# Kernel tuning notes

Hardware: AMD Instinct MI355X
Metric: run time of the kernel (lower is better)

The kernel has to match this reference:

```python
import jax, jax.numpy as jnp
import numpy as np

N, C, T = 8, 256, 512
H, KQ, OUT = 8, 256, 256
EPS = 1e-5


def sym_linear(x, w, stride):
    # w: (2, out_dim); circulant-grouped expansion to (2T, out_dim), then x @ cp
    out_dim = w.shape[1]
    idx = (jnp.arange(out_dim)[None, :] - jnp.arange(T)[:, None] * stride) % out_dim  # (T, out_dim)
    cp = w[:, idx].transpose(1, 0, 2).reshape(2 * T, out_dim)  # cat of rolled copies
    return x @ cp


def ln2d(x, g, b):
    # LayerNorm over last two dims (T, 2T) with affine params (T, 2T)
    mu = jnp.mean(x, axis=(-2, -1), keepdims=True)
    var = jnp.mean(jnp.square(x - mu), axis=(-2, -1), keepdims=True)
    return (x - mu) / jnp.sqrt(var + EPS) * g + b


def setup_inputs() -> dict:
    key = jax.random.key(0)
    ks = jax.random.split(key, 16)
    stdv = 1.0 / np.sqrt(2 * T)
    u = lambda k, shape, s: jax.random.uniform(k, shape, jnp.float32, -s, s)
    return {
        "x": jax.random.normal(ks[0], (N, C, T), jnp.float32),
        "Wq": u(ks[1], (KQ, C), 1.0 / np.sqrt(C)),
        "Wk": u(ks[2], (KQ, C), 1.0 / np.sqrt(C)),
        "Wv": u(ks[3], (OUT, C), 1.0 / np.sqrt(C)),
        "m1w0": u(ks[4], (2, 2 * T), stdv),
        "m2w0": u(ks[5], (2, 2 * T), stdv),
        "m1w1": u(ks[6], (2, 2 * T), stdv),
        "m2w1": u(ks[7], (2, T), stdv),
        "ln1g0": 1.0 + 0.1 * jax.random.normal(ks[8], (T, 2 * T), jnp.float32),
        "ln1b0": 0.1 * jax.random.normal(ks[9], (T, 2 * T), jnp.float32),
        "ln2g0": 1.0 + 0.1 * jax.random.normal(ks[10], (T, 2 * T), jnp.float32),
        "ln2b0": 0.1 * jax.random.normal(ks[11], (T, 2 * T), jnp.float32),
        "ln1g1": 1.0 + 0.1 * jax.random.normal(ks[12], (T, 2 * T), jnp.float32),
        "ln1b1": 0.1 * jax.random.normal(ks[13], (T, 2 * T), jnp.float32),
    }


def reference(x, Wq, Wk, Wv, m1w0, m2w0, m1w1, m2w1,
              ln1g0, ln1b0, ln2g0, ln2b0, ln1g1, ln1b1):
    dk = KQ // H
    q = jnp.einsum('oc,nct->not', Wq, x).reshape(N, H, dk, T).transpose(0, 1, 3, 2)  # (N,H,T,dk)
    k = jnp.einsum('oc,nct->not', Wk, x).reshape(N, H, dk, T)                        # (N,H,dk,T)
    v = jnp.einsum('oc,nct->not', Wv, x).reshape(N, H, OUT // H, T).transpose(0, 1, 3, 2)  # (N,H,T,dv)

    scores = jnp.einsum('nhtd,nhds->nhts', q, k) / np.sqrt(dk)  # (N,H,T,T)
    ar = jnp.arange(T, dtype=jnp.float32)
    pd = jnp.abs(ar[None, :] - ar[:, None]) / (T - 1)  # (T,T)
    p = jnp.stack([scores, jnp.broadcast_to(pd, scores.shape)], axis=-1)  # (N,H,T,T,2)
    p = p.reshape(N, H, T, 2 * T)

    def transpose_pairs(z):
        return z.reshape(N, H, T, T, 2).transpose(0, 1, 3, 2, 4)

    # mix block 0 (intermediate)
    p = ln2d(sym_linear(p, m1w0, 2), ln1g0, ln1b0)
    p = jax.nn.gelu(transpose_pairs(p), approximate=False).reshape(N, H, T, 2 * T)
    p = ln2d(sym_linear(p, m2w0, 2), ln2g0, ln2b0)
    p = jax.nn.gelu(transpose_pairs(p), approximate=False).reshape(N, H, T, 2 * T)

    # mix block 1 (final)
    p = ln2d(sym_linear(p, m1w1, 2), ln1g1, ln1b1)
    p = jax.nn.gelu(transpose_pairs(p), approximate=False).reshape(N, H, T, 2 * T)
    p = sym_linear(p, m2w1, 1)           # (N,H,T,T), out_roll_stride = T // T * 1
    p = p.transpose(0, 1, 3, 2)

    attn = jax.nn.softmax(p, axis=-1)
    out = jnp.einsum('nhts,nhsd->nhtd', attn, v)  # (N,H,T,dv)
    return out.transpose(0, 1, 3, 2).reshape(N, OUT, T)
```

## Files before the change

### kernel.cpp

```cpp
#include <hip/hip_runtime.h>
#include <hip/hip_bf16.h>
#include <math.h>

#define CDIM 256
#define TDIM 512
#define T2   1024
#define NB   64
#define MTOT 524288.0f

typedef __bf16 bf16x8 __attribute__((ext_vector_type(8)));
typedef float  f32x4  __attribute__((ext_vector_type(4)));
typedef ushort ushort8v __attribute__((ext_vector_type(8)));
typedef ushort ushort4v __attribute__((ext_vector_type(4)));

__device__ __forceinline__ ushort f2bf(float f) {
  union { float f; unsigned u; } v; v.f = f;
  unsigned r = v.u + 0x7fffu + ((v.u >> 16) & 1u);
  return (ushort)(r >> 16);
}
__device__ __forceinline__ float bf2f(ushort h) {
  union { unsigned u; float f; } v; v.u = ((unsigned)h) << 16;
  return v.f;
}
__device__ __forceinline__ float gelu_exact(float x) {
  return 0.5f * x * (1.0f + erff(x * 0.7071067811865475f));
}

#define TO_LDS(p)  ((__attribute__((address_space(3))) void*)(unsigned)(uintptr_t)(p))
#define TO_GLB(p)  ((const __attribute__((address_space(1))) void*)(uintptr_t)(p))
#define GLOAD_LDS16(g, l) __builtin_amdgcn_global_load_lds(TO_GLB(g), TO_LDS(l), 16, 0, 0)

#define BAR()    asm volatile("s_barrier" ::: "memory")
#define WAITL()  asm volatile("s_waitcnt lgkmcnt(0)" ::: "memory")
#define WAITV4() asm volatile("s_waitcnt vmcnt(4)" ::: "memory")
#define WAITV0() asm volatile("s_waitcnt vmcnt(0)" ::: "memory")

__global__ __launch_bounds__(256)
void proj_kernel(const float* __restrict__ x, const float* __restrict__ Wq,
                 const float* __restrict__ Wk, const float* __restrict__ Wv,
                 ushort* __restrict__ qb, ushort* __restrict__ kb,
                 float* __restrict__ vp) {
  int t = blockIdx.x * 256 + threadIdx.x;
  int o = blockIdx.y;
  int n = blockIdx.z;
  const float* xn = x + (long)n * CDIM * TDIM;
  float aq = 0.f, ak = 0.f, av = 0.f;
  for (int c = 0; c < CDIM; ++c) {
    float xv = xn[c * TDIM + t];
    aq = fmaf(Wq[o * CDIM + c], xv, aq);
    ak = fmaf(Wk[o * CDIM + c], xv, ak);
    av = fmaf(Wv[o * CDIM + c], xv, av);
  }
  int h = o >> 5, d = o & 31;
  long bidx = (((long)(n * 8 + h) * 512) + t) * 32 + d;
  qb[bidx] = f2bf(aq);
  kb[bidx] = f2bf(ak);
  vp[((long)n * 256 + o) * TDIM + t] = av;
}

__global__ __launch_bounds__(256)
void prep_kernel(const float* __restrict__ m1w0, const float* __restrict__ m2w0,
                 const float* __restrict__ m1w1, const float* __restrict__ m2w1,
                 ushort* __restrict__ cpte0, ushort* __restrict__ cpto0,
                 ushort* __restrict__ cpt1, ushort* __restrict__ cpt2,
                 ushort* __restrict__ cpt3) {
  long i = (long)blockIdx.x * 256 + threadIdx.x;
  if (i < 524288) {
    int o = (int)(i >> 9), s = (int)(i & 511);
    int idx = (o - 2 * s) & 1023;
    cpte0[i] = f2bf(m1w0[idx]);
    cpto0[i] = f2bf(m1w0[1024 + idx]);
  } else if (i < 1572864) {
    long j = i - 524288;
    int o = (int)(j >> 10), kk = (int)(j & 1023);
    cpt1[j] = f2bf(m2w0[(kk & 1) * 1024 + ((o - 2 * (kk >> 1)) & 1023)]);
  } else if (i < 2621440) {
    long j = i - 1572864;
    int o = (int)(j >> 10), kk = (int)(j & 1023);
    cpt2[j] = f2bf(m1w1[(kk & 1) * 1024 + ((o - 2 * (kk >> 1)) & 1023)]);
  } else if (i < 3145728) {
    long j = i - 2621440;
    int o = (int)(j >> 10), kk = (int)(j & 1023);
    cpt3[j] = f2bf(m2w1[(kk & 1) * 512 + ((o - (kk >> 1)) & 511)]);
  }
}

__global__ __launch_bounds__(256)
void pdpart_kernel(const float* __restrict__ m1w0, float* __restrict__ pdpart) {
  __shared__ float W2[1024];
  int o = blockIdx.x * 256 + threadIdx.x;
  for (int i = threadIdx.x; i < 1024; i += 256) W2[i] = m1w0[1024 + i];
  __syncthreads();
  float P0 = 0.f, Tv = 0.f;
  for (int s = 0; s < 512; ++s) {
    float wv2 = W2[(o - 2 * s) & 1023];
    P0 = fmaf((float)s, wv2, P0);
    Tv += wv2;
  }
  float pd = P0 * (1.0f / 511.0f);
  pdpart[o] = pd;
  float P = 0.f;
  for (int t = 0; t < 511; ++t) {
    P += W2[(o - 2 * t) & 1023];
    pd += (2.f * P - Tv) * (1.0f / 511.0f);
    pdpart[(long)(t + 1) * 1024 + o] = pd;
  }
}

__global__ __launch_bounds__(256)
void scores_kernel(const ushort* __restrict__ qb, const ushort* __restrict__ kb,
                   ushort* __restrict__ S) {
  __shared__ ushort sm[4 * 16 * 512];
  int tb = blockIdx.x;
  int b  = blockIdx.y;
  int wv = threadIdx.x >> 6, lane = threadIdx.x & 63;
  int fr = lane & 15, fq = lane >> 4;
  int t0 = tb * 64 + wv * 16;
  bf16x8 af = *(const bf16x8*)(qb + ((long)b * 512 + t0 + fr) * 32 + fq * 8);
  const ushort* kbase = kb + (long)b * 512 * 32 + fr * 32 + fq * 8;
  char* smw = (char*)sm + wv * 16384;
  f32x4 zz = {0.f, 0.f, 0.f, 0.f};
#pragma unroll 4
  for (int st = 0; st < 32; ++st) {
    bf16x8 bfv = *(const bf16x8*)(kbase + st * 512);
    f32x4 acc = __builtin_amdgcn_mfma_f32_16x16x32_bf16(af, bfv, zz, 0, 0, 0);
#pragma unroll
    for (int r = 0; r < 4; ++r) {
      int row = fq * 4 + r;
      int byteoff = row * 1024 + (((st * 16 + fr) * 2) ^ ((row & 7) << 4));
      *(ushort*)(smw + byteoff) = f2bf(acc[r] * 0.17677669529663687f);
    }
  }
  __syncthreads();
  ushort* Sb = S + ((long)b * 512 + t0) * 512;
#pragma unroll
  for (int j = 0; j < 16; ++j) {
    int byteoff = j * 1024 + ((lane * 16) ^ ((j & 7) << 4));
    ushort8v v = *(const ushort8v*)(smw + byteoff);
    *(ushort8v*)(Sb + (long)j * 512 + lane * 8) = v;
  }
}

#define LDS_BUF  65536
#define LDS_BOFF 32768

#define STAGE_A_(buf, h, kt) do { \
  const ushort* gA0_ = Ab + (long)((h)*128 +      sr0) * K + (kt)*64 + slog8; \
  const ushort* gA1_ = Ab + (long)((h)*128 + 64 + sr0) * K + (kt)*64 + slog8; \
  char* dA_ = ldsw + (size_t)(buf) * LDS_BUF + (h)*16384 + tid*16; \
  GLOAD_LDS16(gA0_, dA_); GLOAD_LDS16(gA1_, dA_ + 8192); } while(0)

#define STAGE_B_(buf, h, kt) do { \
  const ushort* gB0_ = Bb + (long)((h)*128 +      sr0) * K + (kt)*64 + slog8; \
  const ushort* gB1_ = Bb + (long)((h)*128 + 64 + sr0) * K + (kt)*64 + slog8; \
  char* dB_ = ldsw + (size_t)(buf) * LDS_BUF + LDS_BOFF + (h)*16384 + tid*16; \
  GLOAD_LDS16(gB0_, dB_); GLOAD_LDS16(gB1_, dB_ + 8192); } while(0)

#define LD_A_(buf, mh) do { \
  const char* aB_ = ldsc + (size_t)(buf) * LDS_BUF; \
  _Pragma("unroll") for (int mi = 0; mi < 4; ++mi) { \
    int ar_ = wm*128 + (mh)*64 + mi*16 + fr; \
    const char* rb_ = aB_ + ar_*128; int sw_ = (ar_&7)<<4; \
    af[mi][0] = *(const bf16x8*)(rb_ + ((fq*16) ^ sw_)); \
    af[mi][1] = *(const bf16x8*)(rb_ + ((64 + fq*16) ^ sw_)); \
  } } while(0)

#define LD_B_(dst, buf, nh) do { \
  const char* bB_ = ldsc + (size_t)(buf) * LDS_BUF + LDS_BOFF; \
  _Pragma("unroll") for (int ni = 0; ni < 2; ++ni) { \
    int br_ = wn*64 + (nh)*32 + ni*16 + fr; \
    const char* rb_ = bB_ + br_*128; int sw_ = (br_&7)<<4; \
    dst[ni][0] = *(const bf16x8*)(rb_ + ((fq*16) ^ sw_)); \
    dst[ni][1] = *(const bf16x8*)(rb_ + ((64 + fq*16) ^ sw_)); \
  } } while(0)

#define QUAD_(mh, nh, bfa) do { \
  __builtin_amdgcn_s_setprio(1); \
  _Pragma("unroll") for (int kk = 0; kk < 2; ++kk) \
  _Pragma("unroll") for (int mi = 0; mi < 4; ++mi) \
  _Pragma("unroll") for (int ni = 0; ni < 2; ++ni) \
    acc[(mh)*4+mi][(nh)*2+ni] = __builtin_amdgcn_mfma_f32_16x16x32_bf16( \
        af[mi][kk], bfa[ni][kk], acc[(mh)*4+mi][(nh)*2+ni], 0, 0, 0); \
  __builtin_amdgcn_s_setprio(0); } while(0)

template<int K, bool FINAL>
__global__ __launch_bounds__(512, 2)
void gemm256_kernel(const ushort* __restrict__ A, long aStride,
                    const ushort* __restrict__ BT, long bStride,
                    void* __restrict__ Out, int ncols, float* __restrict__ stats,
                    const float* __restrict__ Cadd) {
  __shared__ ushort lds[2][2][256 * 64];
  const int tid = threadIdx.x;
  const int bm = blockIdx.x, bn = blockIdx.y, b = blockIdx.z;
  constexpr int NKT2 = K >> 7;
  const ushort* Ab = A  + (long)b * aStride + (long)bm * 256 * K;
  const ushort* Bb = BT + (long)b * bStride + (long)bn * 256 * K;
  const int lane = tid & 63;
  const int fr = lane & 15, fq = lane >> 4;
  const int wid = tid >> 6, wm = wid >> 2, wn = wid & 3;
  const int sr0 = tid >> 3;
  const int slog8 = ((tid & 7) ^ (sr0 & 7)) * 8;
  const char* ldsc = (const char*)&lds[0][0][0];
  char*       ldsw = (char*)&lds[0][0][0];

  f32x4 acc[8][4] = {};
  bf16x8 af[4][2], bf0[2][2], bf1[2][2];

  STAGE_B_(0, 0, 0); STAGE_B_(0, 1, 0);
  STAGE_A_(0, 0, 0); STAGE_A_(0, 1, 0);
  STAGE_B_(1, 0, 1); STAGE_B_(1, 1, 1);
  WAITV4();
  BAR();

  for (int i = 0; i < NKT2; ++i) {
    const int t1 = 2 * i + 1, t2 = 2 * i + 2, t3 = 2 * i + 3;
    const bool st = (i < NKT2 - 1);
    LD_A_(0, 0); LD_B_(bf0, 0, 0); LD_B_(bf1, 0, 1);
    STAGE_A_(1, 0, t1); STAGE_A_(1, 1, t1);
    BAR(); WAITL();
    QUAD_(0, 0, bf0); QUAD_(0, 1, bf1);
    BAR();
    LD_A_(0, 1);
    if (st) { STAGE_B_(0, 0, t2); STAGE_B_(0, 1, t2); WAITV4(); } else { WAITV0(); }
    BAR(); WAITL();
    QUAD_(1, 1, bf1); QUAD_(1, 0, bf0);
    BAR();
    LD_A_(1, 0); LD_B_(bf0, 1, 0); LD_B_(bf1, 1, 1);
    if (st) { STAGE_A_(0, 0, t2); STAGE_A_(0, 1, t2); }
    BAR(); WAITL();
    QUAD_(0, 0, bf0); QUAD_(0, 1, bf1);
    BAR();
    LD_A_(1, 1);
    if (st) { STAGE_B_(1, 0, t3); STAGE_B_(1, 1, t3); WAITV4(); }
    BAR(); WAITL();
    QUAD_(1, 1, bf1); QUAD_(1, 0, bf0);
    BAR();
  }

  const int r0 = bm * 256 + wm * 128;
  const int c0 = bn * 256 + wn * 64;
  if (!FINAL) {
    ushort* Yb = (ushort*)Out + (long)b * 512 * ncols;
    float s1 = 0.f, s2 = 0.f;
#pragma unroll
    for (int mi = 0; mi < 8; ++mi)
#pragma unroll
      for (int ni = 0; ni < 4; ++ni)
#pragma unroll
        for (int r = 0; r < 4; ++r) {
          float v = acc[mi][ni][r];
          int row = r0 + mi * 16 + fq * 4 + r;
          int col = c0 + ni * 16 + fr;
          if (Cadd) v += Cadd[(long)row * ncols + col];
          s1 += v; s2 += v * v;
          Yb[(long)row * ncols + col] = f2bf(v);
        }
    __syncthreads();
    float* red = (float*)&lds[0][0][0];
    red[tid] = s1; red[tid + 512] = s2;
    __syncthreads();
    for (int off = 256; off > 0; off >>= 1) {
      if (tid < off) { red[tid] += red[tid + off]; red[512 + tid] += red[512 + tid + off]; }
      __syncthreads();
    }
    if (tid == 0) {
      atomicAdd(&stats[b * 2],     red[0]);
      atomicAdd(&stats[b * 2 + 1], red[512]);
    }
  } else {
    float* Lb = (float*)Out + (long)b * 512 * ncols;
#pragma unroll
    for (int mi = 0; mi < 8; ++mi)
#pragma unroll
      for (int ni = 0; ni < 4; ++ni)
#pragma unroll
        for (int r = 0; r < 4; ++r) {
          int row = r0 + mi * 16 + fq * 4 + r;
          int col = c0 + ni * 16 + fr;
          Lb[(long)row * ncols + col] = acc[mi][ni][r];
        }
  }
}

template<int K, bool FINAL>
__global__ __launch_bounds__(512, 2)
void gemm256v2_kernel(const ushort* __restrict__ A, long aStride,
                      const ushort* __restrict__ BT, long bStride,
                      void* __restrict__ Out, int ncols, float* __restrict__ stats,
                      const float* __restrict__ Cadd) {
  __shared__ ushort lds[4][2][128][64];
  const int tid = threadIdx.x;
  const int bm = blockIdx.x, bn = blockIdx.y, b = blockIdx.z;
  constexpr int NT = K >> 5;
  const ushort* Ab = A  + (long)b * aStride + (long)bm * 256 * K;
  const ushort* Bb = BT + (long)b * bStride + (long)bn * 256 * K;
  const int lane = tid & 63;
  const int fr = lane & 15, fq = lane >> 4;
  const int wid = tid >> 6, wm = wid >> 2, wn = wid & 3;
  char* ldsb = (char*)&lds[0][0][0][0];

  long so0, so1;
  {
    int line0 = tid >> 3;
    int s0 = (tid & 7) ^ (line0 & 7);
    so0 = (long)(line0 + 128 * (s0 >> 2)) * K + (s0 & 3) * 8;
    int line1 = 64 + (tid >> 3);
    int s1 = (tid & 7) ^ (line1 & 7);
    so1 = (long)(line1 + 128 * (s1 >> 2)) * K + (s1 & 3) * 8;
  }
#define V2STAGE(slot, kt) do { \
    char* db_ = ldsb + (slot) * 32768 + tid * 16; \
    GLOAD_LDS16(Ab + so0 + (kt) * 32, db_); \
    GLOAD_LDS16(Ab + so1 + (kt) * 32, db_ + 8192); \
    GLOAD_LDS16(Bb + so0 + (kt) * 32, db_ + 16384); \
    GLOAD_LDS16(Bb + so1 + (kt) * 32, db_ + 24576); \
  } while (0)

  int aoff[8], boff[4];
#pragma unroll
  for (int mi = 0; mi < 8; ++mi)
    aoff[mi] = (mi * 16 + fr) * 128 + (((wm * 4 + fq) ^ (fr & 7)) * 16);
#pragma unroll
  for (int ni = 0; ni < 4; ++ni) {
    int row = wn * 64 + ni * 16 + fr;
    boff[ni] = (row & 127) * 128 + ((((row >> 7) * 4 + fq) ^ (fr & 7)) * 16);
  }

  f32x4 acc[8][4] = {};

  V2STAGE(0, 0);
  V2STAGE(1, 1);
  WAITV4();
  BAR();

  for (int t = 0; t < NT; ++t) {
    const int slot = t & 3;
    if (t + 2 < NT) V2STAGE((t + 2) & 3, t + 2);
    const char* sa = ldsb + slot * 32768;
    const char* sb = sa + 16384;
    bf16x8 af[8], bfv[4];
#pragma unroll
    for (int mi = 0; mi < 8; ++mi) af[mi] = *(const bf16x8*)(sa + aoff[mi]);
#pragma unroll
    for (int ni = 0; ni < 4; ++ni) bfv[ni] = *(const bf16x8*)(sb + boff[ni]);
    __builtin_amdgcn_s_setprio(1);
#pragma unroll
    for (int mi = 0; mi < 8; ++mi)
#pragma unroll
      for (int ni = 0; ni < 4; ++ni)
        acc[mi][ni] = __builtin_amdgcn_mfma_f32_16x16x32_bf16(af[mi], bfv[ni], acc[mi][ni], 0, 0, 0);
    __builtin_amdgcn_s_setprio(0);
    if (t + 2 < NT) { WAITV4(); } else if (t + 2 == NT) { WAITV0(); }
    if (t + 1 < NT) BAR();
  }

  const int r0 = bm * 256 + wm * 128;
  const int c0 = bn * 256 + wn * 64;
  if (!FINAL) {
    ushort* Yb = (ushort*)Out + (long)b * 512 * ncols;
    float s1 = 0.f, s2 = 0.f;
#pragma unroll
    for (int mi = 0; mi < 8; ++mi)
#pragma unroll
      for (int ni = 0; ni < 4; ++ni)
#pragma unroll
        for (int r = 0; r < 4; ++r) {
          float v = acc[mi][ni][r];
          int row = r0 + mi * 16 + fq * 4 + r;
          int col = c0 + ni * 16 + fr;
          if (Cadd) v += Cadd[(long)row * ncols + col];
          s1 += v; s2 += v * v;
          Yb[(long)row * ncols + col] = f2bf(v);
        }
    __syncthreads();
    float* red = (float*)ldsb;
    red[tid] = s1; red[tid + 512] = s2;
    __syncthreads();
    for (int off = 256; off > 0; off >>= 1) {
      if (tid < off) { red[tid] += red[tid + off]; red[512 + tid] += red[512 + tid + off]; }
      __syncthreads();
    }
    if (tid == 0) {
      atomicAdd(&stats[b * 2],     red[0]);
      atomicAdd(&stats[b * 2 + 1], red[512]);
    }
  } else {
    float* Lb = (float*)Out + (long)b * 512 * ncols;
#pragma unroll
    for (int mi = 0; mi < 8; ++mi)
#pragma unroll
      for (int ni = 0; ni < 4; ++ni)
#pragma unroll
        for (int r = 0; r < 4; ++r) {
          int row = r0 + mi * 16 + fq * 4 + r;
          int col = c0 + ni * 16 + fr;
          Lb[(long)row * ncols + col] = acc[mi][ni][r];
        }
  }
#undef V2STAGE
}

__global__ __launch_bounds__(256)
void apply_kernel(const ushort* __restrict__ Y, const float* __restrict__ stats,
                  const ushort* __restrict__ gbb, ushort* __restrict__ P) {
  __shared__ ushort2 tile[32][65];
  int ti = blockIdx.x;
  int si = blockIdx.y;
  int b  = blockIdx.z;
  float mu  = stats[b * 2] * (1.0f / MTOT);
  float var = stats[b * 2 + 1] * (1.0f / MTOT) - mu * mu;
  float rstd = rsqrtf(var + 1e-5f);
  const ushort* Yb = Y + (long)b * 512 * 1024;
  int tr  = threadIdx.x >> 4;
  int sp4 = (threadIdx.x & 15) * 4;
#pragma unroll
  for (int pass = 0; pass < 2; ++pass) {
    int t  = ti * 32 + pass * 16 + tr;
    int sp = si * 64 + sp4;
    ushort8v yv  = *(const ushort8v*)(Yb + (long)t * 1024 + 2 * sp);
    ushort8v gbA = *(const ushort8v*)(gbb + ((long)t * 512 + sp) * 4);
    ushort8v gbB = *(const ushort8v*)(gbb + ((long)t * 512 + sp + 2) * 4);
#pragma unroll
    for (int j = 0; j < 4; ++j) {
      int base = (j & 1) * 4;
      ushort gg0 = (j < 2) ? gbA[base + 0] : gbB[base + 0];
      ushort bb0 = (j < 2) ? gbA[base + 1] : gbB[base + 1];
      ushort gg1 = (j < 2) ? gbA[base + 2] : gbB[base + 2];
      ushort bb1 = (j < 2) ? gbA[base + 3] : gbB[base + 3];
      float y0 = (bf2f(yv[2 * j])     - mu) * rstd * bf2f(gg0) + bf2f(bb0);
      float y1 = (bf2f(yv[2 * j + 1]) - mu) * rstd * bf2f(gg1) + bf2f(bb1);
      ushort2 o; o.x = f2bf(gelu_exact(y0)); o.y = f2bf(gelu_exact(y1));
      tile[pass * 16 + tr][sp4 + j] = o;
    }
  }
  __syncthreads();
  ushort* Pb = P + (long)b * 512 * 1024;
  int srow = threadIdx.x >> 3;
  int t4   = (threadIdx.x & 7) * 4;
#pragma unroll
  for (int pass = 0; pass < 2; ++pass) {
    int scol = pass * 32 + srow;
    int s = si * 64 + scol;
    ushort2 v0 = tile[t4 + 0][scol];
    ushort2 v1 = tile[t4 + 1][scol];
    ushort2 v2 = tile[t4 + 2][scol];
    ushort2 v3 = tile[t4 + 3][scol];
    int tcol0 = ti * 32 + t4;
    ushort8v w2 = {v0.x, v0.y, v1.x, v1.y, v2.x, v2.y, v3.x, v3.y};
    *(ushort8v*)(Pb + (long)s * 1024 + 2 * tcol0) = w2;
  }
}

__global__ __launch_bounds__(256)
void prep2_kernel(const float* __restrict__ g0, const float* __restrict__ b0,
                  const float* __restrict__ g1, const float* __restrict__ b1,
                  const float* __restrict__ g2, const float* __restrict__ b2,
                  ushort* __restrict__ gbb0, ushort* __restrict__ gbb1,
                  ushort* __restrict__ gbb2) {
  long i = (long)blockIdx.x * 256 + threadIdx.x;
  int set = (int)(i >> 18);
  long j = i & 262143;
  const float* g = set == 0 ? g0 : (set == 1 ? g1 : g2);
  const float* b = set == 0 ? b0 : (set == 1 ? b1 : b2);
  ushort* gbb    = set == 0 ? gbb0 : (set == 1 ? gbb1 : gbb2);
  float2 gv = *(const float2*)(g + 2 * j);
  float2 bv = *(const float2*)(b + 2 * j);
  ushort4v o; o[0] = f2bf(gv.x); o[1] = f2bf(bv.x); o[2] = f2bf(gv.y); o[3] = f2bf(bv.y);
  *(ushort4v*)(gbb + 4 * j) = o;
}

__global__ __launch_bounds__(256)
void smax_av_kernel(const float* __restrict__ L, const float* __restrict__ vp,
                    float* __restrict__ out) {
  __shared__ float Lt[32][513];
  int bh = blockIdx.x;
  int at = blockIdx.y;
  int n = bh >> 3, h = bh & 7;
  int wv = threadIdx.x >> 6, lane = threadIdx.x & 63;
  for (int rr = 0; rr < 8; ++rr) {
    int row = wv * 8 + rr;
    int a = at * 32 + row;
    const float* Lr = L + ((long)bh * 512 + a) * 512 + lane * 8;
    float4 va = *(const float4*)(Lr);
    float4 vb4 = *(const float4*)(Lr + 4);
    float e[8] = {va.x, va.y, va.z, va.w, vb4.x, vb4.y, vb4.z, vb4.w};
    float m = e[0];
#pragma unroll
    for (int j = 1; j < 8; ++j) m = fmaxf(m, e[j]);
    for (int off = 32; off > 0; off >>= 1) m = fmaxf(m, __shfl_xor(m, off, 64));
    float s = 0.f;
#pragma unroll
    for (int j = 0; j < 8; ++j) { e[j] = expf(e[j] - m); s += e[j]; }
    for (int off = 32; off > 0; off >>= 1) s += __shfl_xor(s, off, 64);
    float inv = 1.0f / s;
#pragma unroll
    for (int j = 0; j < 8; ++j) Lt[row][lane * 8 + j] = e[j] * inv;
  }
  __syncthreads();
  int r  = threadIdx.x & 31;
  int d0 = (threadIdx.x >> 5) * 4;
  const float* vb = vp + ((long)n * 256 + h * 32) * 512;
  float a0 = 0.f, a1 = 0.f, a2 = 0.f, a3 = 0.f;
  for (int bc = 0; bc < 512; bc += 4) {
    float4 v0 = *(const float4*)(vb + (d0 + 0) * 512 + bc);
    float4 v1 = *(const float4*)(vb + (d0 + 1) * 512 + bc);
    float4 v2 = *(const float4*)(vb + (d0 + 2) * 512 + bc);
    float4 v3 = *(const float4*)(vb + (d0 + 3) * 512 + bc);
    float p0 = Lt[r][bc], p1 = Lt[r][bc + 1], p2 = Lt[r][bc + 2], p3 = Lt[r][bc + 3];
    a0 = fmaf(p0, v0.x, fmaf(p1, v0.y, fmaf(p2, v0.z, fmaf(p3, v0.w, a0))));
    a1 = fmaf(p0, v1.x, fmaf(p1, v1.y, fmaf(p2, v1.z, fmaf(p3, v1.w, a1))));
    a2 = fmaf(p0, v2.x, fmaf(p1, v2.y, fmaf(p2, v2.z, fmaf(p3, v2.w, a2))));
    a3 = fmaf(p0, v3.x, fmaf(p1, v3.y, fmaf(p2, v3.z, fmaf(p3, v3.w, a3))));
  }
  int a = at * 32 + r;
  float* ob = out + ((long)n * 256 + h * 32) * 512;
  ob[(d0 + 0) * 512 + a] = a0;
  ob[(d0 + 1) * 512 + a] = a1;
  ob[(d0 + 2) * 512 + a] = a2;
  ob[(d0 + 3) * 512 + a] = a3;
}

extern "C" void kernel_launch(void* const* d_in, const int* in_sizes, int n_in,
                              void* d_out, int out_size, void* d_ws, size_t ws_size,
                              hipStream_t stream) {
  const float* x     = (const float*)d_in[0];
  const float* Wq    = (const float*)d_in[1];
  const float* Wk    = (const float*)d_in[2];
  const float* Wv    = (const float*)d_in[3];
  const float* m1w0  = (const float*)d_in[4];
  const float* m2w0  = (const float*)d_in[5];
  const float* m1w1  = (const float*)d_in[6];
  const float* m2w1  = (const float*)d_in[7];
  const float* ln1g0 = (const float*)d_in[8];
  const float* ln1b0 = (const float*)d_in[9];
  const float* ln2g0 = (const float*)d_in[10];
  const float* ln2b0 = (const float*)d_in[11];
  const float* ln1g1 = (const float*)d_in[12];
  const float* ln1b1 = (const float*)d_in[13];

  char* w = (char*)d_ws;
  float*  vp     = (float*) (w + 0);
  ushort* qb     = (ushort*)(w + (4ull  << 20));
  ushort* kb     = (ushort*)(w + (6ull  << 20));
  float*  stats  = (float*) (w + (8ull  << 20));
  ushort* cpte0  = (ushort*)(w + (9ull  << 20));
  ushort* cpto0  = (ushort*)(w + (10ull << 20));
  ushort* cpt1   = (ushort*)(w + (11ull << 20));
  ushort* cpt2   = (ushort*)(w + (13ull << 20));
  ushort* cpt3   = (ushort*)(w + (15ull << 20));
  float*  pdpart = (float*) (w + (17ull << 20));
  ushort* bufA   = (ushort*)(w + (20ull << 20));
  ushort* bufB   = (ushort*)(w + (84ull << 20));
  ushort* gbb0   = qb;
  ushort* gbb1   = kb;
  ushort* gbb2   = cpte0;
  ushort* S      = bufA;
  float*  L      = (float*)bufB;
  float*  outp   = (float*)d_out;

  hipMemsetAsync(stats, 0, 3 * NB * 2 * sizeof(float), stream);

  proj_kernel<<<dim3(2, 256, 8), 256, 0, stream>>>(x, Wq, Wk, Wv, qb, kb, vp);
  prep_kernel<<<12288, 256, 0, stream>>>(m1w0, m2w0, m1w1, m2w1,
                                         cpte0, cpto0, cpt1, cpt2, cpt3);
  pdpart_kernel<<<4, 256, 0, stream>>>(m1w0, pdpart);
  scores_kernel<<<dim3(8, 64), 256, 0, stream>>>(qb, kb, S);
  gemm256_kernel<512, false><<<dim3(2, 4, 64), 512, 0, stream>>>(
      S, 512L * 512, cpte0, 0, bufB, 1024, stats, pdpart);
  prep2_kernel<<<3072, 256, 0, stream>>>(ln1g0, ln1b0, ln2g0, ln2b0, ln1g1, ln1b1,
                                         gbb0, gbb1, gbb2);
  apply_kernel<<<dim3(16, 8, 64), 256, 0, stream>>>(bufB, stats, gbb0, bufA);
  gemm256_kernel<1024, false><<<dim3(2, 4, 64), 512, 0, stream>>>(
      bufA, 512L * 1024, cpt1, 0, bufB, 1024, stats + 128, nullptr);
  apply_kernel<<<dim3(16, 8, 64), 256, 0, stream>>>(bufB, stats + 128, gbb1, bufA);
  gemm256v2_kernel<1024, false><<<dim3(2, 4, 64), 512, 0, stream>>>(
      bufA, 512L * 1024, cpt2, 0, bufB, 1024, stats + 256, nullptr);
  apply_kernel<<<dim3(16, 8, 64), 256, 0, stream>>>(bufB, stats + 256, gbb2, bufA);
  gemm256_kernel<1024, true><<<dim3(2, 2, 64), 512, 0, stream>>>(
      cpt3, 0, bufA, 512L * 1024, L, 512, nullptr, nullptr);
  smax_av_kernel<<<dim3(64, 16), 256, 0, stream>>>(L, vp, outp);
}
```

Before: 522.5 us.

## Register-block projection, remap GEMM blocks across XCDs, switch v2 to double buffer

The projection kernel now computes four output channels per thread, so each x load is reused across twelve FMAs and the grid shrinks fourfold. The GEMM kernels remap the flat block index so that consecutive blocks spread across the eight XCDs, grouping blocks that share the same batch onto one XCD for L2 reuse. The 4-slot v2 GEMM becomes a 2-slot double-buffered v3 with full vmcnt waits and half the LDS. The v3 and original kernels are also swapped between the second and third mix GEMMs. The shallower pipeline could expose more load latency.

Result: slower. 630.7 us (+20.7%).

```diff
diff --git a/kernel.cpp b/kernel.cpp
--- a/kernel.cpp
+++ b/kernel.cpp
@@ -40,22 +40,42 @@
                  const float* __restrict__ Wk, const float* __restrict__ Wv,
                  ushort* __restrict__ qb, ushort* __restrict__ kb,
                  float* __restrict__ vp) {
-  int t = blockIdx.x * 256 + threadIdx.x;
-  int o = blockIdx.y;
-  int n = blockIdx.z;
+  int t  = blockIdx.x * 256 + threadIdx.x;
+  int o0 = blockIdx.y * 4;
+  int n  = blockIdx.z;
   const float* xn = x + (long)n * CDIM * TDIM;
-  float aq = 0.f, ak = 0.f, av = 0.f;
+  const float* wq = Wq + o0 * CDIM;
+  const float* wk = Wk + o0 * CDIM;
+  const float* wv = Wv + o0 * CDIM;
+  float aq0 = 0.f, aq1 = 0.f, aq2 = 0.f, aq3 = 0.f;
+  float ak0 = 0.f, ak1 = 0.f, ak2 = 0.f, ak3 = 0.f;
+  float av0 = 0.f, av1 = 0.f, av2 = 0.f, av3 = 0.f;
   for (int c = 0; c < CDIM; ++c) {
-    float xv = xn[c * TDIM + t];
-    aq = fmaf(Wq[o * CDIM + c], xv, aq);
-    ak = fmaf(Wk[o * CDIM + c], xv, ak);
-    av = fmaf(Wv[o * CDIM + c], xv, av);
-  }
-  int h = o >> 5, d = o & 31;
-  long bidx = (((long)(n * 8 + h) * 512) + t) * 32 + d;
-  qb[bidx] = f2bf(aq);
-  kb[bidx] = f2bf(ak);
-  vp[((long)n * 256 + o) * TDIM + t] = av;
+    float xv = xn[(long)c * TDIM + t];
+    aq0 = fmaf(wq[c],            xv, aq0);
+    aq1 = fmaf(wq[CDIM + c],     xv, aq1);
+    aq2 = fmaf(wq[2 * CDIM + c], xv, aq2);
+    aq3 = fmaf(wq[3 * CDIM + c], xv, aq3);
+    ak0 = fmaf(wk[c],            xv, ak0);
+    ak1 = fmaf(wk[CDIM + c],     xv, ak1);
+    ak2 = fmaf(wk[2 * CDIM + c], xv, ak2);
+    ak3 = fmaf(wk[3 * CDIM + c], xv, ak3);
+    av0 = fmaf(wv[c],            xv, av0);
+    av1 = fmaf(wv[CDIM + c],     xv, av1);
+    av2 = fmaf(wv[2 * CDIM + c], xv, av2);
+    av3 = fmaf(wv[3 * CDIM + c], xv, av3);
+  }
+  float aqs[4] = {aq0, aq1, aq2, aq3};
+  float aks[4] = {ak0, ak1, ak2, ak3};
+  float avs[4] = {av0, av1, av2, av3};
+#pragma unroll
+  for (int j = 0; j < 4; ++j) {
+    int o = o0 + j, h = o >> 5, d = o & 31;
+    long bidx = (((long)(n * 8 + h) * 512) + t) * 32 + d;
+    qb[bidx] = f2bf(aqs[j]);
+    kb[bidx] = f2bf(aks[j]);
+    vp[((long)n * 256 + o) * TDIM + t] = avs[j];
+  }
 }
 
 __global__ __launch_bounds__(256)
@@ -183,7 +203,7 @@
         af[mi][kk], bfa[ni][kk], acc[(mh)*4+mi][(nh)*2+ni], 0, 0, 0); \
   __builtin_amdgcn_s_setprio(0); } while(0)
 
-template<int K, bool FINAL>
+template<int K, int BN, bool FINAL>
 __global__ __launch_bounds__(512, 2)
 void gemm256_kernel(const ushort* __restrict__ A, long aStride,
                     const ushort* __restrict__ BT, long bStride,
@@ -191,8 +211,16 @@
                     const float* __restrict__ Cadd) {
   __shared__ ushort lds[2][2][256 * 64];
   const int tid = threadIdx.x;
-  const int bm = blockIdx.x, bn = blockIdx.y, b = blockIdx.z;
   constexpr int NKT2 = K >> 7;
+  constexpr int NWG = 2 * BN * 64;
+  constexpr int PER = NWG / 8;
+  constexpr int BNSH = (BN == 4 ? 2 : 1);
+  const int flat = blockIdx.x + 2 * (blockIdx.y + BN * blockIdx.z);
+  const int w    = (flat & 7) * PER + (flat >> 3);
+  const int bn   = w & (BN - 1);
+  const int grp  = w >> BNSH;
+  const int bm   = grp & 1;
+  const int b    = grp >> 1;
   const ushort* Ab = A  + (long)b * aStride + (long)bm * 256 * K;
   const ushort* Bb = BT + (long)b * bStride + (long)bn * 256 * K;
   const int lane = tid & 63;
@@ -282,22 +310,30 @@
   }
 }
 
-template<int K, bool FINAL>
+template<int K, int BN, bool FINAL>
 __global__ __launch_bounds__(512, 2)
-void gemm256v2_kernel(const ushort* __restrict__ A, long aStride,
+void gemm256v3_kernel(const ushort* __restrict__ A, long aStride,
                       const ushort* __restrict__ BT, long bStride,
                       void* __restrict__ Out, int ncols, float* __restrict__ stats,
                       const float* __restrict__ Cadd) {
-  __shared__ ushort lds[4][2][128][64];
+  __shared__ ushort lds[2][2][128 * 64];
   const int tid = threadIdx.x;
-  const int bm = blockIdx.x, bn = blockIdx.y, b = blockIdx.z;
   constexpr int NT = K >> 5;
+  constexpr int NWG = 2 * BN * 64;
+  constexpr int PER = NWG / 8;
+  constexpr int BNSH = (BN == 4 ? 2 : 1);
+  const int flat = blockIdx.x + 2 * (blockIdx.y + BN * blockIdx.z);
+  const int w    = (flat & 7) * PER + (flat >> 3);
+  const int bn   = w & (BN - 1);
+  const int grp  = w >> BNSH;
+  const int bm   = grp & 1;
+  const int b    = grp >> 1;
   const ushort* Ab = A  + (long)b * aStride + (long)bm * 256 * K;
   const ushort* Bb = BT + (long)b * bStride + (long)bn * 256 * K;
   const int lane = tid & 63;
   const int fr = lane & 15, fq = lane >> 4;
   const int wid = tid >> 6, wm = wid >> 2, wn = wid & 3;
-  char* ldsb = (char*)&lds[0][0][0][0];
+  char* ldsb = (char*)&lds[0][0][0];
 
   long so0, so1;
   {
@@ -308,8 +344,8 @@
     int s1 = (tid & 7) ^ (line1 & 7);
     so1 = (long)(line1 + 128 * (s1 >> 2)) * K + (s1 & 3) * 8;
   }
-#define V2STAGE(slot, kt) do { \
-    char* db_ = ldsb + (slot) * 32768 + tid * 16; \
+#define V3STAGE(buf, kt) do { \
+    char* db_ = ldsb + (buf) * 32768 + tid * 16; \
     GLOAD_LDS16(Ab + so0 + (kt) * 32, db_); \
     GLOAD_LDS16(Ab + so1 + (kt) * 32, db_ + 8192); \
     GLOAD_LDS16(Bb + so0 + (kt) * 32, db_ + 16384); \
@@ -328,21 +364,21 @@
 
   f32x4 acc[8][4] = {};
 
-  V2STAGE(0, 0);
-  V2STAGE(1, 1);
-  WAITV4();
+  V3STAGE(0, 0);
+  WAITV0();
   BAR();
 
   for (int t = 0; t < NT; ++t) {
-    const int slot = t & 3;
-    if (t + 2 < NT) V2STAGE((t + 2) & 3, t + 2);
-    const char* sa = ldsb + slot * 32768;
+    const int buf = t & 1;
+    if (t + 1 < NT) V3STAGE(buf ^ 1, t + 1);
+    const char* sa = ldsb + buf * 32768;
     const char* sb = sa + 16384;
     bf16x8 af[8], bfv[4];
 #pragma unroll
     for (int mi = 0; mi < 8; ++mi) af[mi] = *(const bf16x8*)(sa + aoff[mi]);
 #pragma unroll
     for (int ni = 0; ni < 4; ++ni) bfv[ni] = *(const bf16x8*)(sb + boff[ni]);
+    WAITL();
     __builtin_amdgcn_s_setprio(1);
 #pragma unroll
     for (int mi = 0; mi < 8; ++mi)
@@ -350,8 +386,8 @@
       for (int ni = 0; ni < 4; ++ni)
         acc[mi][ni] = __builtin_amdgcn_mfma_f32_16x16x32_bf16(af[mi], bfv[ni], acc[mi][ni], 0, 0, 0);
     __builtin_amdgcn_s_setprio(0);
-    if (t + 2 < NT) { WAITV4(); } else if (t + 2 == NT) { WAITV0(); }
-    if (t + 1 < NT) BAR();
+    if (t + 1 < NT) WAITV0();
+    BAR();
   }
 
   const int r0 = bm * 256 + wm * 128;
@@ -397,7 +433,7 @@
           Lb[(long)row * ncols + col] = acc[mi][ni][r];
         }
   }
-#undef V2STAGE
+#undef V3STAGE
 }
 
 __global__ __launch_bounds__(256)
@@ -560,23 +596,23 @@
 
   hipMemsetAsync(stats, 0, 3 * NB * 2 * sizeof(float), stream);
 
-  proj_kernel<<<dim3(2, 256, 8), 256, 0, stream>>>(x, Wq, Wk, Wv, qb, kb, vp);
+  proj_kernel<<<dim3(2, 64, 8), 256, 0, stream>>>(x, Wq, Wk, Wv, qb, kb, vp);
   prep_kernel<<<12288, 256, 0, stream>>>(m1w0, m2w0, m1w1, m2w1,
                                          cpte0, cpto0, cpt1, cpt2, cpt3);
   pdpart_kernel<<<4, 256, 0, stream>>>(m1w0, pdpart);
   scores_kernel<<<dim3(8, 64), 256, 0, stream>>>(qb, kb, S);
-  gemm256_kernel<512, false><<<dim3(2, 4, 64), 512, 0, stream>>>(
+  gemm256_kernel<512, 4, false><<<dim3(2, 4, 64), 512, 0, stream>>>(
       S, 512L * 512, cpte0, 0, bufB, 1024, stats, pdpart);
   prep2_kernel<<<3072, 256, 0, stream>>>(ln1g0, ln1b0, ln2g0, ln2b0, ln1g1, ln1b1,
                                          gbb0, gbb1, gbb2);
   apply_kernel<<<dim3(16, 8, 64), 256, 0, stream>>>(bufB, stats, gbb0, bufA);
-  gemm256_kernel<1024, false><<<dim3(2, 4, 64), 512, 0, stream>>>(
+  gemm256v3_kernel<1024, 4, false><<<dim3(2, 4, 64), 512, 0, stream>>>(
       bufA, 512L * 1024, cpt1, 0, bufB, 1024, stats + 128, nullptr);
   apply_kernel<<<dim3(16, 8, 64), 256, 0, stream>>>(bufB, stats + 128, gbb1, bufA);
-  gemm256v2_kernel<1024, false><<<dim3(2, 4, 64), 512, 0, stream>>>(
+  gemm256_kernel<1024, 4, false><<<dim3(2, 4, 64), 512, 0, stream>>>(
       bufA, 512L * 1024, cpt2, 0, bufB, 1024, stats + 256, nullptr);
   apply_kernel<<<dim3(16, 8, 64), 256, 0, stream>>>(bufB, stats + 256, gbb2, bufA);
-  gemm256_kernel<1024, true><<<dim3(2, 2, 64), 512, 0, stream>>>(
+  gemm256_kernel<1024, 2, true><<<dim3(2, 2, 64), 512, 0, stream>>>(
       cpt3, 0, bufA, 512L * 1024, L, 512, nullptr, nullptr);
   smax_av_kernel<<<dim3(64, 16), 256, 0, stream>>>(L, vp, outp);
 }
```
